# Performance work log

Hardware: AMD Instinct MI355X
Metric: run time of the kernel (lower is better)

## Reference

```python
import jax, jax.numpy as jnp
import numpy as np

N_HEADS = 16
HEAD_DIM = 64
EMB = 1024
B, S = 2, 2048


def setup_inputs() -> dict:
    key = jax.random.key(0)
    ks = jax.random.split(key, 8)
    inner = N_HEADS * HEAD_DIM
    return {
        "query": jax.random.normal(ks[0], (B, S, EMB), dtype=jnp.float32),
        "key": jax.random.normal(ks[1], (B, S, EMB), dtype=jnp.float32),
        "value": jax.random.normal(ks[2], (B, S, EMB), dtype=jnp.float32),
        "positional_mask": jnp.ones((B, S), dtype=bool),
        "future_mask": 1,
        # torch nn.Linear weight layout: (out_features, in_features)
        "Wq": jax.random.normal(ks[3], (inner, EMB), dtype=jnp.float32) * 0.02,
        "Wk": jax.random.normal(ks[4], (inner, EMB), dtype=jnp.float32) * 0.02,
        "Wv": jax.random.normal(ks[5], (inner, EMB), dtype=jnp.float32) * 0.02,
        "Wo": jax.random.normal(ks[6], (EMB, inner), dtype=jnp.float32) * 0.02,
        "bo": jax.random.normal(ks[7], (EMB,), dtype=jnp.float32) * 0.02,
    }


def reference(query, key, value, positional_mask, future_mask, Wq, Wk, Wv, Wo, bo):
    batch, seq = query.shape[:2]
    # project and split heads: (B, S, H, D)
    q = (query @ Wq.T).reshape(batch, seq, N_HEADS, HEAD_DIM)
    k = (key @ Wk.T).reshape(batch, seq, N_HEADS, HEAD_DIM)
    v = (value @ Wv.T).reshape(batch, seq, N_HEADS, HEAD_DIM)
    scale = 1.0 / np.sqrt(HEAD_DIM).astype(np.float32)
    # (B, H, Sq, Sk)
    weights = jnp.einsum("bqhd,bkhd->bhqk", q, k) * scale
    neg_inf = jnp.float32(-jnp.inf)
    # additive key-position mask
    reweight = jnp.where(positional_mask, jnp.float32(0.0), neg_inf)  # (B, S)
    weights = weights + reweight[:, None, None, :]
    if future_mask:
        causal = jnp.triu(jnp.full((seq, seq), neg_inf, dtype=weights.dtype), k=1)
        weights = weights + causal
    weights = jax.nn.softmax(weights, axis=-1)
    out = jnp.einsum("bhqk,bkhd->bqhd", weights, v).reshape(batch, seq, -1)
    return out @ Wo.T + bo
```

## Files before the change

kernel.cpp:

```cpp
#include <hip/hip_runtime.h>
#include <hip/hip_bf16.h>
#include <math.h>

#define EMB    1024
#define NH     16
#define HD     64
#define BATCH  2
#define SEQ    2048
#define MTOK   (BATCH * SEQ)

typedef __bf16 bf16_t;
typedef __bf16 bf16x8 __attribute__((ext_vector_type(8)));
typedef __bf16 bf16x4 __attribute__((ext_vector_type(4)));
typedef float  f32x4  __attribute__((ext_vector_type(4)));

#define NEG_BIG (-1.0e30f)

#define GLD16(g, l) __builtin_amdgcn_global_load_lds(                     \
    (const __attribute__((address_space(1))) void*)(g),                   \
    (__attribute__((address_space(3))) void*)(l), 16, 0, 0)

__device__ inline bf16x8 ld_frag64(const bf16_t* __restrict__ p) {
    const bf16x4 lo = *(const bf16x4*)p;
    const bf16x4 hi = *(const bf16x4*)(p + 4);
    bf16x8 r;
#pragma unroll
    for (int j = 0; j < 4; ++j) { r[j] = lo[j]; r[j + 4] = hi[j]; }
    return r;
}

__global__ __launch_bounds__(256) void cast_bf16(
    const float* __restrict__ q, const float* __restrict__ k,
    const float* __restrict__ v, const float* __restrict__ wq,
    const float* __restrict__ wk, const float* __restrict__ wv,
    const float* __restrict__ wo, bf16_t* __restrict__ ws)
{
    const size_t g = ((size_t)blockIdx.x * 256 + threadIdx.x) * 8;
    const size_t BIG = (size_t)1 << 22;
    const size_t SML = (size_t)1 << 20;
    const float* src;
    bf16_t* dst;
    size_t off;
    if (g < 3 * BIG) {
        const int s = (int)(g >> 22);
        src = s == 0 ? q : (s == 1 ? k : v);
        dst = ws + (size_t)s * BIG;
        off = g & (BIG - 1);
    } else {
        const size_t h = g - 3 * BIG;
        const int s = (int)(h >> 20);
        src = s == 0 ? wq : (s == 1 ? wk : (s == 2 ? wv : wo));
        dst = ws + 3 * BIG + (size_t)s * SML;
        off = h & (SML - 1);
    }
    const f32x4 f0 = *(const f32x4*)(src + off);
    const f32x4 f1 = *(const f32x4*)(src + off + 4);
    bf16x8 r;
#pragma unroll
    for (int j = 0; j < 4; ++j) { r[j] = (bf16_t)f0[j]; r[j + 4] = (bf16_t)f1[j]; }
    *(bf16x8*)(dst + off) = r;
}

template<int BM, int BN, bool OUTF32>
__global__ __launch_bounds__(256) void gemm_dma(
    const bf16_t* __restrict__ A, const bf16_t* __restrict__ Wb,
    const float* __restrict__ bias, void* __restrict__ Cp,
    size_t sA, size_t sW, size_t sC)
{
    constexpr int K = EMB, N = EMB;
    constexpr int MT = BM / 32, NT = BN / 32;
    constexpr int IA = BM / 64, IB = BN / 64;
    __shared__ __align__(16) bf16_t As[2][BM * 32];
    __shared__ __align__(16) bf16_t Bs[2][BN * 32];

    const int tid  = threadIdx.x;
    const int wave = tid >> 6;
    const int lane = tid & 63;
    const int l15  = lane & 15;
    const int quad = lane >> 4;
    const int z    = blockIdx.z;
    A  += (size_t)z * sA;
    Wb += (size_t)z * sW;

    const int m0 = blockIdx.y * BM;
    const int n0 = blockIdx.x * BN;
    const int wm = (wave >> 1) * (BM / 2);
    const int wn = (wave & 1) * (BN / 2);

    const int lrow = lane >> 2;
    const int scol = ((lane & 3) ^ (lrow & 3)) * 8;
    const bf16_t* gA = A  + (size_t)(m0 + wave * (BM / 4) + lrow) * K + scol;
    const bf16_t* gB = Wb + (size_t)(n0 + wave * (BN / 4) + lrow) * K + scol;
    const int loffA = wave * (BM / 4) * 32;
    const int loffB = wave * (BN / 4) * 32;

    f32x4 acc[MT][NT] = {};

    const int xq = (quad ^ (l15 & 3)) * 8;

#pragma unroll
    for (int i = 0; i < IA; ++i) GLD16(gA + (size_t)i * 16 * K, &As[0][loffA + i * 512]);
#pragma unroll
    for (int i = 0; i < IB; ++i) GLD16(gB + (size_t)i * 16 * K, &Bs[0][loffB + i * 512]);

    for (int t = 0; t < K / 32; ++t) {
        __syncthreads();
        if (t + 1 < K / 32) {
            const size_t ko = (size_t)(t + 1) * 32;
            const int nb = (t + 1) & 1;
#pragma unroll
            for (int i = 0; i < IA; ++i)
                GLD16(gA + ko + (size_t)i * 16 * K, &As[nb][loffA + i * 512]);
#pragma unroll
            for (int i = 0; i < IB; ++i)
                GLD16(gB + ko + (size_t)i * 16 * K, &Bs[nb][loffB + i * 512]);
        }
        const int buf = t & 1;
        bf16x8 af[MT], bfr[NT];
#pragma unroll
        for (int mt = 0; mt < MT; ++mt)
            af[mt] = *(const bf16x8*)&As[buf][(wm + mt * 16 + l15) * 32 + xq];
#pragma unroll
        for (int nt = 0; nt < NT; ++nt)
            bfr[nt] = *(const bf16x8*)&Bs[buf][(wn + nt * 16 + l15) * 32 + xq];
#pragma unroll
        for (int mt = 0; mt < MT; ++mt)
#pragma unroll
            for (int nt = 0; nt < NT; ++nt)
                acc[mt][nt] = __builtin_amdgcn_mfma_f32_16x16x32_bf16(
                    af[mt], bfr[nt], acc[mt][nt], 0, 0, 0);
    }

    const size_t cb = (size_t)z * sC;
#pragma unroll
    for (int nt = 0; nt < NT; ++nt) {
        const int col = n0 + wn + nt * 16 + l15;
        const float bv = bias ? bias[col] : 0.0f;
#pragma unroll
        for (int mt = 0; mt < MT; ++mt) {
#pragma unroll
            for (int r = 0; r < 4; ++r) {
                const int row = m0 + wm + mt * 16 + quad * 4 + r;
                const float v = acc[mt][nt][r] + bv;
                if constexpr (OUTF32) ((float*) Cp)[cb + (size_t)row * N + col] = v;
                else                  ((bf16_t*)Cp)[cb + (size_t)row * N + col] = (bf16_t)v;
            }
        }
    }
}

__global__ __launch_bounds__(256) void attn_flash(
    const bf16_t* __restrict__ Q, const bf16_t* __restrict__ Km,
    const bf16_t* __restrict__ V, bf16_t* __restrict__ O)
{
    __shared__ __align__(16) bf16_t Ks[32][72];
    __shared__ bf16_t Vs[64][36];
    __shared__ bf16_t Pb[4][16 * 40];
    __shared__ bf16_t Ob[4][16 * 72];

    const int tid  = threadIdx.x;
    const int wave = tid >> 6;
    const int lane = tid & 63;
    const int l15  = lane & 15;
    const int quad = lane >> 4;
    const int b = blockIdx.z, h = blockIdx.y;
    const int qi = gridDim.x - 1 - blockIdx.x;
    const int qbase = qi * 64 + wave * 16;

    const bf16_t* Qb = Q  + ((size_t)b * SEQ) * EMB + h * HD;
    const bf16_t* Kb = Km + ((size_t)b * SEQ) * EMB + h * HD;
    const bf16_t* Vb = V  + ((size_t)b * SEQ) * EMB + h * HD;

    const int tr = tid >> 3;
    const int tc = (tid & 7) * 8;
    const int vk = wave * 8;

    const bf16x8 qlo = *(const bf16x8*)(Qb + (size_t)(qbase + l15) * EMB + quad * 8);
    const bf16x8 qhi = *(const bf16x8*)(Qb + (size_t)(qbase + l15) * EMB + 32 + quad * 8);

    float m_s = NEG_BIG, l_s = 0.0f;
    f32x4 o[4] = {};
    const float scale = 0.125f;
    const int qg = qbase + l15;

    bf16_t* P = Pb[wave];
    const int nkt = qi * 2 + 2;

    for (int kt = 0; kt < nkt; ++kt) {
        const int kb = kt * 32;

        {
            const bf16x8 kv = *(const bf16x8*)(Kb + (size_t)(kb + tr) * EMB + tc);
            *(bf16x8*)&Ks[tr][tc] = kv;
            bf16x4 v0, v1;
#pragma unroll
            for (int j = 0; j < 4; ++j)
                v0[j] = Vb[(size_t)(kb + vk + j) * EMB + lane];
#pragma unroll
            for (int j = 0; j < 4; ++j)
                v1[j] = Vb[(size_t)(kb + vk + 4 + j) * EMB + lane];
            *(bf16x4*)&Vs[lane][vk]     = v0;
            *(bf16x4*)&Vs[lane][vk + 4] = v1;
        }
        __syncthreads();

        const bf16x8 k0lo = *(const bf16x8*)&Ks[l15][quad * 8];
        const bf16x8 k0hi = *(const bf16x8*)&Ks[l15][32 + quad * 8];
        const bf16x8 k1lo = *(const bf16x8*)&Ks[16 + l15][quad * 8];
        const bf16x8 k1hi = *(const bf16x8*)&Ks[16 + l15][32 + quad * 8];

        f32x4 s0 = {}, s1 = {};
        __builtin_amdgcn_s_setprio(1);
        s0 = __builtin_amdgcn_mfma_f32_16x16x32_bf16(k0lo, qlo, s0, 0, 0, 0);
        s0 = __builtin_amdgcn_mfma_f32_16x16x32_bf16(k0hi, qhi, s0, 0, 0, 0);
        s1 = __builtin_amdgcn_mfma_f32_16x16x32_bf16(k1lo, qlo, s1, 0, 0, 0);
        s1 = __builtin_amdgcn_mfma_f32_16x16x32_bf16(k1hi, qhi, s1, 0, 0, 0);
        __builtin_amdgcn_s_setprio(0);

        float v[8];
#pragma unroll
        for (int r = 0; r < 4; ++r) {
            v[r]     = (kb + quad * 4 + r      > qg) ? NEG_BIG : s0[r] * scale;
            v[4 + r] = (kb + 16 + quad * 4 + r > qg) ? NEG_BIG : s1[r] * scale;
        }
        float mx = v[0];
#pragma unroll
        for (int j = 1; j < 8; ++j) mx = fmaxf(mx, v[j]);
        mx = fmaxf(mx, __shfl_xor(mx, 16, 64));
        mx = fmaxf(mx, __shfl_xor(mx, 32, 64));
        const float mnew  = fmaxf(m_s, mx);
        const float alpha = __expf(m_s - mnew);
        float e[8], rs = 0.0f;
#pragma unroll
        for (int j = 0; j < 8; ++j) { e[j] = __expf(v[j] - mnew); rs += e[j]; }
        rs += __shfl_xor(rs, 16, 64);
        rs += __shfl_xor(rs, 32, 64);
        l_s = l_s * alpha + rs;
        m_s = mnew;
#pragma unroll
        for (int dt = 0; dt < 4; ++dt)
#pragma unroll
            for (int r = 0; r < 4; ++r) o[dt][r] *= alpha;

        bf16x4 p0, p1;
#pragma unroll
        for (int r = 0; r < 4; ++r) { p0[r] = (bf16_t)e[r]; p1[r] = (bf16_t)e[4 + r]; }
        *(bf16x4*)&P[l15 * 40 + quad * 4]      = p0;
        *(bf16x4*)&P[l15 * 40 + 16 + quad * 4] = p1;
        __asm__ volatile("s_waitcnt lgkmcnt(0)" ::: "memory");
        const bf16x8 pb = ld_frag64(&P[l15 * 40 + quad * 8]);

        __builtin_amdgcn_s_setprio(1);
#pragma unroll
        for (int dt = 0; dt < 4; ++dt) {
            const bf16x8 va = ld_frag64(&Vs[dt * 16 + l15][quad * 8]);
            o[dt] = __builtin_amdgcn_mfma_f32_16x16x32_bf16(va, pb, o[dt], 0, 0, 0);
        }
        __builtin_amdgcn_s_setprio(0);
        __syncthreads();
    }

    const float inv = 1.0f / l_s;
    bf16_t* OT = Ob[wave];
#pragma unroll
    for (int dt = 0; dt < 4; ++dt) {
        bf16x4 pk;
#pragma unroll
        for (int r = 0; r < 4; ++r) pk[r] = (bf16_t)(o[dt][r] * inv);
        *(bf16x4*)&OT[l15 * 72 + dt * 16 + quad * 4] = pk;
    }
    __asm__ volatile("s_waitcnt lgkmcnt(0)" ::: "memory");
    const bf16x8 r0 = *(const bf16x8*)&OT[l15 * 72 + quad * 16];
    const bf16x8 r1 = *(const bf16x8*)&OT[l15 * 72 + quad * 16 + 8];
    bf16_t* dst = O + ((size_t)b * SEQ + qbase + l15) * EMB + h * HD + quad * 16;
    *(bf16x8*)dst       = r0;
    *(bf16x8*)(dst + 8) = r1;
}

extern "C" void kernel_launch(void* const* d_in, const int* in_sizes, int n_in,
                              void* d_out, int out_size, void* d_ws, size_t ws_size,
                              hipStream_t stream)
{
    const float* query = (const float*)d_in[0];
    const float* key   = (const float*)d_in[1];
    const float* value = (const float*)d_in[2];
    const float* Wq = (const float*)d_in[5];
    const float* Wk = (const float*)d_in[6];
    const float* Wv = (const float*)d_in[7];
    const float* Wo = (const float*)d_in[8];
    const float* bo = (const float*)d_in[9];

    const size_t BIG = (size_t)1 << 22, SML = (size_t)1 << 20;
    bf16_t* ws  = (bf16_t*)d_ws;
    bf16_t* qc  = ws;
    bf16_t* kc  = qc + BIG;
    bf16_t* vc  = kc + BIG;
    bf16_t* wqc = vc + BIG;
    bf16_t* wkc = wqc + SML;
    bf16_t* wvc = wkc + SML;
    bf16_t* woc = wvc + SML;
    bf16_t* Qp  = woc + SML;
    bf16_t* Kp  = Qp + BIG;
    bf16_t* Vp  = Kp + BIG;
    bf16_t* Ab  = Vp + BIG;

    const dim3 blk(256);

    cast_bf16<<<dim3(8192), blk, 0, stream>>>(query, key, value, Wq, Wk, Wv, Wo, ws);

    gemm_dma<128, 128, false><<<dim3(EMB / 128, MTOK / 128, 3), blk, 0, stream>>>(
        qc, wqc, nullptr, Qp, BIG, SML, BIG);

    attn_flash<<<dim3(SEQ / 64, NH, BATCH), blk, 0, stream>>>(Qp, Kp, Vp, Ab);

    gemm_dma<64, 128, true><<<dim3(EMB / 128, MTOK / 64, 1), blk, 0, stream>>>(
        Ab, woc, bo, (float*)d_out, 0, 0, 0);
}
```

Measured before the change: 280.0 us.

## Restructure causal flash attention with 64-key tiles, paired query blocks, and lazy rescaling

The attention kernel now processes 64-key tiles instead of 32, loading K through global_load_lds into a swizzled LDS layout. Each block handles two query tiles (i and 31-i) so causal work is balanced across blocks, and the grid is halved. The causal mask is applied only on the diagonal tile, and the online-softmax rescale is skipped unless the running max grows by more than a threshold. This cuts per-tile sync and softmax overhead, but lowers block count and parallelism and raises register and LDS use.

New measurement: 241.4 us. -13.8%, faster.

```diff
diff --git a/kernel.cpp b/kernel.cpp
--- a/kernel.cpp
+++ b/kernel.cpp
@@ -95,7 +95,6 @@
     const int loffB = wave * (BN / 4) * 32;
 
     f32x4 acc[MT][NT] = {};
-
     const int xq = (quad ^ (l15 & 3)) * 8;
 
 #pragma unroll
@@ -153,9 +152,9 @@
     const bf16_t* __restrict__ Q, const bf16_t* __restrict__ Km,
     const bf16_t* __restrict__ V, bf16_t* __restrict__ O)
 {
-    __shared__ __align__(16) bf16_t Ks[32][72];
-    __shared__ bf16_t Vs[64][36];
-    __shared__ bf16_t Pb[4][16 * 40];
+    __shared__ __align__(16) bf16_t Ks[64 * 64];
+    __shared__ __align__(16) bf16_t Vs[64][76];
+    __shared__ bf16_t Pb[4][16 * 68];
     __shared__ bf16_t Ob[4][16 * 72];
 
     const int tid  = threadIdx.x;
@@ -164,117 +163,137 @@
     const int l15  = lane & 15;
     const int quad = lane >> 4;
     const int b = blockIdx.z, h = blockIdx.y;
-    const int qi = gridDim.x - 1 - blockIdx.x;
-    const int qbase = qi * 64 + wave * 16;
 
     const bf16_t* Qb = Q  + ((size_t)b * SEQ) * EMB + h * HD;
     const bf16_t* Kb = Km + ((size_t)b * SEQ) * EMB + h * HD;
     const bf16_t* Vb = V  + ((size_t)b * SEQ) * EMB + h * HD;
 
-    const int tr = tid >> 3;
-    const int tc = (tid & 7) * 8;
-    const int vk = wave * 8;
-
-    const bf16x8 qlo = *(const bf16x8*)(Qb + (size_t)(qbase + l15) * EMB + quad * 8);
-    const bf16x8 qhi = *(const bf16x8*)(Qb + (size_t)(qbase + l15) * EMB + 32 + quad * 8);
-
-    float m_s = NEG_BIG, l_s = 0.0f;
-    f32x4 o[4] = {};
+    const int krow = lane >> 3;
+    const int kcol = ((lane & 7) ^ krow) * 8;
+    const int vk   = wave * 16;
+    bf16_t* P = Pb[wave];
     const float scale = 0.125f;
-    const int qg = qbase + l15;
-
-    bf16_t* P = Pb[wave];
-    const int nkt = qi * 2 + 2;
-
-    for (int kt = 0; kt < nkt; ++kt) {
-        const int kb = kt * 32;
-
-        {
-            const bf16x8 kv = *(const bf16x8*)(Kb + (size_t)(kb + tr) * EMB + tc);
-            *(bf16x8*)&Ks[tr][tc] = kv;
-            bf16x4 v0, v1;
-#pragma unroll
-            for (int j = 0; j < 4; ++j)
-                v0[j] = Vb[(size_t)(kb + vk + j) * EMB + lane];
-#pragma unroll
-            for (int j = 0; j < 4; ++j)
-                v1[j] = Vb[(size_t)(kb + vk + 4 + j) * EMB + lane];
-            *(bf16x4*)&Vs[lane][vk]     = v0;
-            *(bf16x4*)&Vs[lane][vk + 4] = v1;
+    const int sw = l15 & 7;
+
+    for (int ph = 0; ph < 2; ++ph) {
+        const int qi = (ph == 0) ? (int)blockIdx.x : 31 - (int)blockIdx.x;
+        const int qbase = qi * 64 + wave * 16;
+        const int qg = qbase + l15;
+        const int nkt = qi + 1;
+
+        const bf16x8 qlo = *(const bf16x8*)(Qb + (size_t)(qbase + l15) * EMB + quad * 8);
+        const bf16x8 qhi = *(const bf16x8*)(Qb + (size_t)(qbase + l15) * EMB + 32 + quad * 8);
+
+        float m_s = NEG_BIG, l_s = 0.0f;
+        f32x4 o[4] = {};
+
+        for (int kt = 0; kt < nkt; ++kt) {
+            const int kb = kt * 64;
+
+#pragma unroll
+            for (int i = 0; i < 2; ++i) {
+                const int r0 = wave * 16 + i * 8;
+                GLD16(Kb + (size_t)(kb + r0 + krow) * EMB + kcol, &Ks[r0 * 64]);
+            }
+#pragma unroll
+            for (int t = 0; t < 4; ++t) {
+                bf16x4 vv;
+#pragma unroll
+                for (int j = 0; j < 4; ++j)
+                    vv[j] = Vb[(size_t)(kb + vk + t * 4 + j) * EMB + lane];
+                *(bf16x4*)&Vs[lane][vk + t * 4] = vv;
+            }
+            __syncthreads();
+
+            f32x4 s[4];
+            __builtin_amdgcn_s_setprio(1);
+#pragma unroll
+            for (int t2 = 0; t2 < 4; ++t2) {
+                const int row = t2 * 16 + l15;
+                const bf16x8 klo = *(const bf16x8*)&Ks[row * 64 + ((quad ^ sw) * 8)];
+                const bf16x8 khi = *(const bf16x8*)&Ks[row * 64 + (((4 + quad) ^ sw) * 8)];
+                f32x4 a = {};
+                a = __builtin_amdgcn_mfma_f32_16x16x32_bf16(klo, qlo, a, 0, 0, 0);
+                a = __builtin_amdgcn_mfma_f32_16x16x32_bf16(khi, qhi, a, 0, 0, 0);
+                s[t2] = a;
+            }
+            __builtin_amdgcn_s_setprio(0);
+
+            float sc[16];
+#pragma unroll
+            for (int t2 = 0; t2 < 4; ++t2)
+#pragma unroll
+                for (int r = 0; r < 4; ++r)
+                    sc[t2 * 4 + r] = s[t2][r] * scale;
+            if (kt == nkt - 1) {
+#pragma unroll
+                for (int t2 = 0; t2 < 4; ++t2)
+#pragma unroll
+                    for (int r = 0; r < 4; ++r)
+                        if (kb + t2 * 16 + quad * 4 + r > qg)
+                            sc[t2 * 4 + r] = NEG_BIG;
+            }
+            float mx = sc[0];
+#pragma unroll
+            for (int j = 1; j < 16; ++j) mx = fmaxf(mx, sc[j]);
+            mx = fmaxf(mx, __shfl_xor(mx, 16, 64));
+            mx = fmaxf(mx, __shfl_xor(mx, 32, 64));
+            if (!__all(mx - m_s <= 8.0f)) {
+                const float mnew  = fmaxf(m_s, mx);
+                const float alpha = __expf(m_s - mnew);
+                l_s *= alpha;
+#pragma unroll
+                for (int dt = 0; dt < 4; ++dt)
+#pragma unroll
+                    for (int r = 0; r < 4; ++r) o[dt][r] *= alpha;
+                m_s = mnew;
+            }
+            float e[16], rs = 0.0f;
+#pragma unroll
+            for (int j = 0; j < 16; ++j) { e[j] = __expf(sc[j] - m_s); rs += e[j]; }
+            rs += __shfl_xor(rs, 16, 64);
+            rs += __shfl_xor(rs, 32, 64);
+            l_s += rs;
+
+#pragma unroll
+            for (int t2 = 0; t2 < 4; ++t2) {
+                bf16x4 p4;
+#pragma unroll
+                for (int r = 0; r < 4; ++r) p4[r] = (bf16_t)e[t2 * 4 + r];
+                *(bf16x4*)&P[l15 * 68 + t2 * 16 + quad * 4] = p4;
+            }
+            __asm__ volatile("s_waitcnt lgkmcnt(0)" ::: "memory");
+            const bf16x8 pb0 = ld_frag64(&P[l15 * 68 + quad * 8]);
+            const bf16x8 pb1 = ld_frag64(&P[l15 * 68 + 32 + quad * 8]);
+
+            __builtin_amdgcn_s_setprio(1);
+#pragma unroll
+            for (int dt = 0; dt < 4; ++dt) {
+                const bf16x8 va0 = ld_frag64(&Vs[dt * 16 + l15][quad * 8]);
+                const bf16x8 va1 = ld_frag64(&Vs[dt * 16 + l15][32 + quad * 8]);
+                o[dt] = __builtin_amdgcn_mfma_f32_16x16x32_bf16(va0, pb0, o[dt], 0, 0, 0);
+                o[dt] = __builtin_amdgcn_mfma_f32_16x16x32_bf16(va1, pb1, o[dt], 0, 0, 0);
+            }
+            __builtin_amdgcn_s_setprio(0);
+            __syncthreads();
         }
-        __syncthreads();
-
-        const bf16x8 k0lo = *(const bf16x8*)&Ks[l15][quad * 8];
-        const bf16x8 k0hi = *(const bf16x8*)&Ks[l15][32 + quad * 8];
-        const bf16x8 k1lo = *(const bf16x8*)&Ks[16 + l15][quad * 8];
-        const bf16x8 k1hi = *(const bf16x8*)&Ks[16 + l15][32 + quad * 8];
-
-        f32x4 s0 = {}, s1 = {};
-        __builtin_amdgcn_s_setprio(1);
-        s0 = __builtin_amdgcn_mfma_f32_16x16x32_bf16(k0lo, qlo, s0, 0, 0, 0);
-        s0 = __builtin_amdgcn_mfma_f32_16x16x32_bf16(k0hi, qhi, s0, 0, 0, 0);
-        s1 = __builtin_amdgcn_mfma_f32_16x16x32_bf16(k1lo, qlo, s1, 0, 0, 0);
-        s1 = __builtin_amdgcn_mfma_f32_16x16x32_bf16(k1hi, qhi, s1, 0, 0, 0);
-        __builtin_amdgcn_s_setprio(0);
-
-        float v[8];
-#pragma unroll
-        for (int r = 0; r < 4; ++r) {
-            v[r]     = (kb + quad * 4 + r      > qg) ? NEG_BIG : s0[r] * scale;
-            v[4 + r] = (kb + 16 + quad * 4 + r > qg) ? NEG_BIG : s1[r] * scale;
+
+        const float inv = 1.0f / l_s;
+        bf16_t* OT = Ob[wave];
+#pragma unroll
+        for (int dt = 0; dt < 4; ++dt) {
+            bf16x4 pk;
+#pragma unroll
+            for (int r = 0; r < 4; ++r) pk[r] = (bf16_t)(o[dt][r] * inv);
+            *(bf16x4*)&OT[l15 * 72 + dt * 16 + quad * 4] = pk;
         }
-        float mx = v[0];
-#pragma unroll
-        for (int j = 1; j < 8; ++j) mx = fmaxf(mx, v[j]);
-        mx = fmaxf(mx, __shfl_xor(mx, 16, 64));
-        mx = fmaxf(mx, __shfl_xor(mx, 32, 64));
-        const float mnew  = fmaxf(m_s, mx);
-        const float alpha = __expf(m_s - mnew);
-        float e[8], rs = 0.0f;
-#pragma unroll
-        for (int j = 0; j < 8; ++j) { e[j] = __expf(v[j] - mnew); rs += e[j]; }
-        rs += __shfl_xor(rs, 16, 64);
-        rs += __shfl_xor(rs, 32, 64);
-        l_s = l_s * alpha + rs;
-        m_s = mnew;
-#pragma unroll
-        for (int dt = 0; dt < 4; ++dt)
-#pragma unroll
-            for (int r = 0; r < 4; ++r) o[dt][r] *= alpha;
-
-        bf16x4 p0, p1;
-#pragma unroll
-        for (int r = 0; r < 4; ++r) { p0[r] = (bf16_t)e[r]; p1[r] = (bf16_t)e[4 + r]; }
-        *(bf16x4*)&P[l15 * 40 + quad * 4]      = p0;
-        *(bf16x4*)&P[l15 * 40 + 16 + quad * 4] = p1;
         __asm__ volatile("s_waitcnt lgkmcnt(0)" ::: "memory");
-        const bf16x8 pb = ld_frag64(&P[l15 * 40 + quad * 8]);
-
-        __builtin_amdgcn_s_setprio(1);
-#pragma unroll
-        for (int dt = 0; dt < 4; ++dt) {
-            const bf16x8 va = ld_frag64(&Vs[dt * 16 + l15][quad * 8]);
-            o[dt] = __builtin_amdgcn_mfma_f32_16x16x32_bf16(va, pb, o[dt], 0, 0, 0);
-        }
-        __builtin_amdgcn_s_setprio(0);
-        __syncthreads();
+        const bf16x8 r0 = *(const bf16x8*)&OT[l15 * 72 + quad * 16];
+        const bf16x8 r1 = *(const bf16x8*)&OT[l15 * 72 + quad * 16 + 8];
+        bf16_t* dst = O + ((size_t)b * SEQ + qbase + l15) * EMB + h * HD + quad * 16;
+        *(bf16x8*)dst       = r0;
+        *(bf16x8*)(dst + 8) = r1;
     }
-
-    const float inv = 1.0f / l_s;
-    bf16_t* OT = Ob[wave];
-#pragma unroll
-    for (int dt = 0; dt < 4; ++dt) {
-        bf16x4 pk;
-#pragma unroll
-        for (int r = 0; r < 4; ++r) pk[r] = (bf16_t)(o[dt][r] * inv);
-        *(bf16x4*)&OT[l15 * 72 + dt * 16 + quad * 4] = pk;
-    }
-    __asm__ volatile("s_waitcnt lgkmcnt(0)" ::: "memory");
-    const bf16x8 r0 = *(const bf16x8*)&OT[l15 * 72 + quad * 16];
-    const bf16x8 r1 = *(const bf16x8*)&OT[l15 * 72 + quad * 16 + 8];
-    bf16_t* dst = O + ((size_t)b * SEQ + qbase + l15) * EMB + h * HD + quad * 16;
-    *(bf16x8*)dst       = r0;
-    *(bf16x8*)(dst + 8) = r1;
 }
 
 extern "C" void kernel_launch(void* const* d_in, const int* in_sizes, int n_in,
@@ -311,7 +330,7 @@
     gemm_dma<128, 128, false><<<dim3(EMB / 128, MTOK / 128, 3), blk, 0, stream>>>(
         qc, wqc, nullptr, Qp, BIG, SML, BIG);
 
-    attn_flash<<<dim3(SEQ / 64, NH, BATCH), blk, 0, stream>>>(Qp, Kp, Vp, Ab);
+    attn_flash<<<dim3(SEQ / 128, NH, BATCH), blk, 0, stream>>>(Qp, Kp, Vp, Ab);
 
     gemm_dma<64, 128, true><<<dim3(EMB / 128, MTOK / 64, 1), blk, 0, stream>>>(
         Ab, woc, bo, (float*)d_out, 0, 0, 0);
```
